# Performance work log

Measured on AMD Instinct MI355X. Metric: run time of the kernel, lower is better.

The kernel has to match this reference:

```python
import jax, jax.numpy as jnp
import numpy as np

N, E = 50000, 300000
NI, EI, H, OUT, L = 16, 8, 64, 3, 3  # node/edge input widths, hidden, output, conv_depth


def setup_inputs() -> dict:
    key = jax.random.key(0)
    ks = iter(jax.random.split(key, 64))
    def rn(shape, scale=0.05):
        return jax.random.normal(next(ks), shape, dtype=jnp.float32) * scale
    inp = {}
    inp["nodes"] = jax.random.normal(next(ks), (N, NI), dtype=jnp.float32)
    inp["edges"] = jax.random.normal(next(ks), (E, EI), dtype=jnp.float32)
    inp["edge_idx"] = jax.random.randint(next(ks), (E, 2), 0, N, dtype=jnp.int32)
    def mlp_params(prefix, din, lead=None):
        s = () if lead is None else (lead,)
        inp[prefix + "_W1"] = rn(s + (din, H))
        inp[prefix + "_b1"] = jnp.zeros(s + (H,), jnp.float32)
        inp[prefix + "_W2"] = rn(s + (H, H))
        inp[prefix + "_b2"] = jnp.zeros(s + (H,), jnp.float32)
        inp[prefix + "_g"] = jnp.ones(s + (H,), jnp.float32)
        inp[prefix + "_be"] = jnp.zeros(s + (H,), jnp.float32)
    mlp_params("ne", NI)            # node encoder
    mlp_params("ee", EI)            # edge encoder
    mlp_params("nm", 2 * H, lead=L)  # node messengers (stacked over conv_depth)
    mlp_params("em", 3 * H, lead=L)  # edge messengers
    inp["dec_W1"] = rn((H, H)); inp["dec_b1"] = jnp.zeros((H,), jnp.float32)
    inp["dec_W2"] = rn((H, OUT)); inp["dec_b2"] = jnp.zeros((OUT,), jnp.float32)
    return inp


def _lrelu(x):
    return jnp.where(x >= 0, x, 0.05 * x)


def _ln(x, g, b):
    m = jnp.mean(x, axis=-1, keepdims=True)
    v = jnp.mean((x - m) ** 2, axis=-1, keepdims=True)
    return (x - m) * jax.lax.rsqrt(v + 1e-5) * g + b


def _mlp(x, W1, b1, W2, b2, g, b):
    h = _lrelu(x @ W1 + b1)
    h = _lrelu(h @ W2 + b2)
    return _ln(h, g, b)


def reference(nodes, edges, edge_idx,
              ne_W1, ne_b1, ne_W2, ne_b2, ne_g, ne_be,
              ee_W1, ee_b1, ee_W2, ee_b2, ee_g, ee_be,
              nm_W1, nm_b1, nm_W2, nm_b2, nm_g, nm_be,
              em_W1, em_b1, em_W2, em_b2, em_g, em_be,
              dec_W1, dec_b1, dec_W2, dec_b2):
    n = _mlp(nodes, ne_W1, ne_b1, ne_W2, ne_b2, ne_g, ne_be)   # [N, H]
    e = _mlp(edges, ee_W1, ee_b1, ee_W2, ee_b2, ee_g, ee_be)   # [E, H]
    s, r = edge_idx[:, 0], edge_idx[:, 1]
    for i in range(L):
        e = e + _mlp(jnp.concatenate([e, n[s], n[r]], axis=1),
                     em_W1[i], em_b1[i], em_W2[i], em_b2[i], em_g[i], em_be[i])
        aggr = jax.ops.segment_sum(e, s, num_segments=n.shape[0])  # scatter_add onto senders
        n = n + _mlp(jnp.concatenate([n, aggr], axis=1),
                     nm_W1[i], nm_b1[i], nm_W2[i], nm_b2[i], nm_g[i], nm_be[i])
    h = _lrelu(n @ dec_W1 + dec_b1)
    return h @ dec_W2 + dec_b2  # [N, OUT]
```

## Files before the change

### kernel.cpp

```cpp
#include <hip/hip_runtime.h>

typedef __attribute__((ext_vector_type(8))) short short8v;
typedef __attribute__((ext_vector_type(4))) short short4v;
typedef __attribute__((ext_vector_type(4))) float f32x4;

__device__ __forceinline__ float lrelu(float x) { return x >= 0.f ? x : 0.05f * x; }

__device__ __forceinline__ unsigned short bf16_rne(float x) {
    unsigned u = __float_as_uint(x);
    u += 0x7FFFu + ((u >> 16) & 1u);
    return (unsigned short)(u >> 16);
}
__device__ __forceinline__ float bf16_to_f(unsigned short h) {
    return __uint_as_float(((unsigned)h) << 16);
}
__device__ __forceinline__ void split2(float x, unsigned short& hi, unsigned short& lo) {
    hi = bf16_rne(x);
    lo = bf16_rne(x - bf16_to_f(hi));
}


__device__ __forceinline__ void stageW(const float* src, int row0, int nrows,
                                       short* __restrict__ A, int wm, int lane)
{
    #pragma unroll
    for (int it = 0; it < 4; ++it) {
        const int q = it * 64 + lane;
        const int rl = wm * 16 + (q >> 4);
        const int k0 = (q & 15) << 2;
        const int grow = row0 + rl;
        float4 x = (grow < nrows) ? *reinterpret_cast<const float4*>(src + (long long)grow * 64 + k0)
                                  : make_float4(0.f, 0.f, 0.f, 0.f);
        unsigned short h0,h1,h2,h3,l0,l1,l2,l3;
        split2(x.x, h0, l0); split2(x.y, h1, l1); split2(x.z, h2, l2); split2(x.w, h3, l3);
        const int off = rl * 64 + ((((k0 >> 3) ^ (rl & 7))) << 3) + (k0 & 7);
        short4v hv; hv[0]=(short)h0; hv[1]=(short)h1; hv[2]=(short)h2; hv[3]=(short)h3;
        short4v lv; lv[0]=(short)l0; lv[1]=(short)l1; lv[2]=(short)l2; lv[3]=(short)l3;
        *reinterpret_cast<short4v*>(A + off) = hv;
        *reinterpret_cast<short4v*>(A + 4096 + off) = lv;
    }
}

__device__ __forceinline__ void gemm64(const short* __restrict__ A, const short* __restrict__ wf,
                                       int row, int g, int lane, f32x4* __restrict__ acc)
{
    #pragma unroll
    for (int s = 0; s < 2; ++s) {
        const int k8 = s * 4 + g;
        const int aoff = row * 64 + ((k8 ^ (row & 7)) << 3);
        const short8v a_hi = *reinterpret_cast<const short8v*>(A + aoff);
        const short8v a_lo = *reinterpret_cast<const short8v*>(A + 4096 + aoff);
        #pragma unroll
        for (int t = 0; t < 4; ++t) {
            const short8v b_hi = *reinterpret_cast<const short8v*>(wf + ((s*4+t)*2+0)*512 + lane*8);
            const short8v b_lo = *reinterpret_cast<const short8v*>(wf + ((s*4+t)*2+1)*512 + lane*8);
            acc[t] = __builtin_amdgcn_mfma_f32_16x16x32_bf16(a_hi, b_hi, acc[t], 0, 0, 0);
            acc[t] = __builtin_amdgcn_mfma_f32_16x16x32_bf16(a_lo, b_hi, acc[t], 0, 0, 0);
            acc[t] = __builtin_amdgcn_mfma_f32_16x16x32_bf16(a_hi, b_lo, acc[t], 0, 0, 0);
        }
    }
}

__device__ __forceinline__ void repackW(short* __restrict__ A, const float4* __restrict__ q,
                                        int wm, int g, int c4)
{
    #pragma unroll
    for (int r = 0; r < 4; ++r) {
        const int rl = wm * 16 + g * 4 + r;
        const int off = rl * 64 + (((c4 >> 3) ^ (rl & 7)) << 3) + (c4 & 7);
        unsigned short h0,h1,h2,h3,l0,l1,l2,l3;
        split2(q[r].x, h0, l0); split2(q[r].y, h1, l1); split2(q[r].z, h2, l2); split2(q[r].w, h3, l3);
        short4v hv; hv[0]=(short)h0; hv[1]=(short)h1; hv[2]=(short)h2; hv[3]=(short)h3;
        short4v lv; lv[0]=(short)l0; lv[1]=(short)l1; lv[2]=(short)l2; lv[3]=(short)l3;
        *reinterpret_cast<short4v*>(A + off) = hv;
        *reinterpret_cast<short4v*>(A + 4096 + off) = lv;
    }
}

__global__ void k_prepw(const float* __restrict__ emW1, const float* __restrict__ emW2,
                        const float* __restrict__ nmW1, const float* __restrict__ nmW2,
                        const float* __restrict__ eeW2, const float* __restrict__ neW2,
                        const float* __restrict__ decW1,
                        short* __restrict__ wf)
{
    const int cid = blockIdx.x;
    const float* src;
    if (cid < 21) {
        const int layer = cid / 7, j = cid % 7;
        src =
            j == 0 ? emW1 + (size_t)layer * 12288 :
            j == 1 ? emW1 + (size_t)layer * 12288 + 4096 :
            j == 2 ? emW1 + (size_t)layer * 12288 + 8192 :
            j == 3 ? emW2 + (size_t)layer * 4096 :
            j == 4 ? nmW1 + (size_t)layer * 8192 :
            j == 5 ? nmW1 + (size_t)layer * 8192 + 4096 :
                     nmW2 + (size_t)layer * 4096;
    } else {
        src = (cid == 21) ? eeW2 : (cid == 22) ? neW2 : decW1;
    }
    short* dst = wf + (size_t)cid * 8192;
    for (int fr = threadIdx.x; fr < 1024; fr += 256) {
        const int lane = fr & 63;
        const int stp = fr >> 6;
        const int p = stp & 1;
        const int st = stp >> 1;
        const int s = st >> 2, t = st & 3;
        const int col = ((lane & 15) << 2) + t;
        const int k0 = s * 32 + (lane >> 4) * 8;
        short8v o;
        #pragma unroll
        for (int i = 0; i < 8; ++i) {
            const float w = src[(k0 + i) * 64 + col];
            const unsigned short hi = bf16_rne(w);
            o[i] = (short)(p ? bf16_rne(w - bf16_to_f(hi)) : hi);
        }
        *reinterpret_cast<short8v*>(dst + fr * 8) = o;
    }
}

template<int DIN, bool PERM, bool MAKEUV, bool OUTBF16>
__global__ __launch_bounds__(256, 4) void k_enc_mf(
    const float* __restrict__ x, const int* __restrict__ csr,
    const float* __restrict__ W1, const float* __restrict__ b1,
    const short* __restrict__ wfW2, const float* __restrict__ b2,
    const float* __restrict__ gam, const float* __restrict__ bet,
    float* __restrict__ out,
    const short* __restrict__ wfB, const short* __restrict__ wfC,
    float* __restrict__ u, float* __restrict__ v, int nrows)
{
    __shared__ short Hf[8192];
    const int row0 = blockIdx.x * 64;
    const int lane = threadIdx.x & 63;
    const int wm = threadIdx.x >> 6;
    const int g = lane >> 4, c = lane & 15;
    const int c4 = c << 2;
    const int rowA = wm * 16 + c;

    long long orig[4];
    #pragma unroll
    for (int r = 0; r < 4; ++r) {
        const int grow = row0 + wm * 16 + g * 4 + r;
        orig[r] = (grow < nrows) ? (long long)(PERM ? csr[grow] : grow) : -1;
    }

    const f32x4 z4 = {0.f, 0.f, 0.f, 0.f};
    f32x4 acc[4];
    #pragma unroll
    for (int t = 0; t < 4; ++t) acc[t] = z4;

    #pragma unroll
    for (int kq = 0; kq < DIN / 4; ++kq) {
        float xv[4][4];
        #pragma unroll
        for (int r = 0; r < 4; ++r) {
            float4 t4 = make_float4(0.f, 0.f, 0.f, 0.f);
            if (orig[r] >= 0)
                t4 = *reinterpret_cast<const float4*>(x + orig[r] * DIN + kq * 4);
            xv[r][0] = t4.x; xv[r][1] = t4.y; xv[r][2] = t4.z; xv[r][3] = t4.w;
        }
        #pragma unroll
        for (int i = 0; i < 4; ++i) {
            const int k = kq * 4 + i;
            const float4 w4 = *reinterpret_cast<const float4*>(W1 + k * 64 + c4);
            const float wv[4] = {w4.x, w4.y, w4.z, w4.w};
            #pragma unroll
            for (int t = 0; t < 4; ++t)
                #pragma unroll
                for (int r = 0; r < 4; ++r)
                    acc[t][r] = fmaf(xv[r][i], wv[t], acc[t][r]);
        }
    }

    const float4 b1q = *reinterpret_cast<const float4*>(b1 + c4);
    float4 hq[4];
    #pragma unroll
    for (int r = 0; r < 4; ++r) {
        hq[r].x = lrelu(acc[0][r] + b1q.x);
        hq[r].y = lrelu(acc[1][r] + b1q.y);
        hq[r].z = lrelu(acc[2][r] + b1q.z);
        hq[r].w = lrelu(acc[3][r] + b1q.w);
    }
    repackW(Hf, hq, wm, g, c4);
    __builtin_amdgcn_wave_barrier();

    f32x4 acc2[4];
    #pragma unroll
    for (int t = 0; t < 4; ++t) acc2[t] = z4;
    gemm64(Hf, wfW2, rowA, g, lane, acc2);

    const float4 b2q = *reinterpret_cast<const float4*>(b2 + c4);
    const float b2a[4] = {b2q.x, b2q.y, b2q.z, b2q.w};
    #pragma unroll
    for (int t = 0; t < 4; ++t) {
        #pragma unroll
        for (int r = 0; r < 4; ++r) acc2[t][r] = lrelu(acc2[t][r] + b2a[t]);
    }
    const float4 gq = *reinterpret_cast<const float4*>(gam + c4);
    const float4 bq = *reinterpret_cast<const float4*>(bet + c4);
    float4 nq[4];
    #pragma unroll
    for (int r = 0; r < 4; ++r) {
        float s = acc2[0][r] + acc2[1][r] + acc2[2][r] + acc2[3][r];
        s += __shfl_xor(s, 1); s += __shfl_xor(s, 2); s += __shfl_xor(s, 4); s += __shfl_xor(s, 8);
        const float mu = s * 0.015625f;
        float q = 0.f;
        #pragma unroll
        for (int t = 0; t < 4; ++t) { const float d = acc2[t][r] - mu; q = fmaf(d, d, q); }
        q += __shfl_xor(q, 1); q += __shfl_xor(q, 2); q += __shfl_xor(q, 4); q += __shfl_xor(q, 8);
        const float rs = rsqrtf(q * 0.015625f + 1e-5f);
        nq[r].x = (acc2[0][r] - mu) * rs * gq.x + bq.x;
        nq[r].y = (acc2[1][r] - mu) * rs * gq.y + bq.y;
        nq[r].z = (acc2[2][r] - mu) * rs * gq.z + bq.z;
        nq[r].w = (acc2[3][r] - mu) * rs * gq.w + bq.w;
        const int grow = row0 + wm * 16 + g * 4 + r;
        if (grow < nrows) {
            if constexpr (OUTBF16) {
                short4v st;
                st[0] = (short)bf16_rne(nq[r].x);
                st[1] = (short)bf16_rne(nq[r].y);
                st[2] = (short)bf16_rne(nq[r].z);
                st[3] = (short)bf16_rne(nq[r].w);
                *reinterpret_cast<short4v*>(reinterpret_cast<unsigned short*>(out) + (long long)grow * 64 + c4) = st;
            } else {
                *reinterpret_cast<float4*>(out + (long long)grow * 64 + c4) = nq[r];
            }
        }
    }

    if constexpr (MAKEUV) {
        repackW(Hf, nq, wm, g, c4);
        __builtin_amdgcn_wave_barrier();
        #pragma unroll
        for (int t = 0; t < 4; ++t) acc2[t] = z4;
        gemm64(Hf, wfB, rowA, g, lane, acc2);
        #pragma unroll
        for (int r = 0; r < 4; ++r) {
            const int grow = row0 + wm * 16 + g * 4 + r;
            if (grow < nrows) {
                float4 o; o.x = acc2[0][r]; o.y = acc2[1][r]; o.z = acc2[2][r]; o.w = acc2[3][r];
                *reinterpret_cast<float4*>(u + (long long)grow * 64 + c4) = o;
            }
        }
        #pragma unroll
        for (int t = 0; t < 4; ++t) acc2[t] = z4;
        gemm64(Hf, wfC, rowA, g, lane, acc2);
        #pragma unroll
        for (int r = 0; r < 4; ++r) {
            const int grow = row0 + wm * 16 + g * 4 + r;
            if (grow < nrows) {
                float4 o; o.x = acc2[0][r]; o.y = acc2[1][r]; o.z = acc2[2][r]; o.w = acc2[3][r];
                *reinterpret_cast<float4*>(v + (long long)grow * 64 + c4) = o;
            }
        }
    }
}

__global__ __launch_bounds__(256, 4) void k_edge_mf(
    unsigned short* ebf, const int* __restrict__ sp, const int* __restrict__ rp,
    const float* __restrict__ u, const float* __restrict__ v,
    const short* __restrict__ wfA, const short* __restrict__ wfW2,
    const float* __restrict__ b1, const float* __restrict__ b2,
    const float* __restrict__ gam, const float* __restrict__ bet, int E)
{
    __shared__ short Hf[8192];
    const int row0 = blockIdx.x * 64;
    const int lane = threadIdx.x & 63;
    const int wm = threadIdx.x >> 6;
    const int g = lane >> 4, c = lane & 15;
    const int c4 = c << 2;
    const int rowA = wm * 16 + c;

    int sidx[4], ridx[4];
    #pragma unroll
    for (int r = 0; r < 4; ++r) {
        const int grow = row0 + wm * 16 + g * 4 + r;
        if (grow < E) { sidx[r] = sp[grow]; ridx[r] = rp[grow]; }
        else          { sidx[r] = 0; ridx[r] = 0; }
    }
    const int arow = (row0 + rowA < E) ? row0 + rowA : 0;
    const short8v a0 = *reinterpret_cast<const short8v*>(ebf + (long long)arow * 64 + g * 8);
    const short8v a1 = *reinterpret_cast<const short8v*>(ebf + (long long)arow * 64 + 32 + g * 8);
    short4v eold[4];
    #pragma unroll
    for (int r = 0; r < 4; ++r) {
        const int grow = row0 + wm * 16 + g * 4 + r;
        const int rc = (grow < E) ? grow : 0;
        eold[r] = *reinterpret_cast<const short4v*>(ebf + (long long)rc * 64 + c4);
    }
    float4 uu[4], vv[4];
    #pragma unroll
    for (int r = 0; r < 4; ++r) {
        uu[r] = *reinterpret_cast<const float4*>(u + (long long)sidx[r] * 64 + c4);
        vv[r] = *reinterpret_cast<const float4*>(v + (long long)ridx[r] * 64 + c4);
    }

    const f32x4 z4 = {0.f, 0.f, 0.f, 0.f};
    f32x4 acc[4];
    #pragma unroll
    for (int t = 0; t < 4; ++t) acc[t] = z4;
    #pragma unroll
    for (int s = 0; s < 2; ++s) {
        const short8v a = s ? a1 : a0;
        #pragma unroll
        for (int t = 0; t < 4; ++t) {
            const short8v b_hi = *reinterpret_cast<const short8v*>(wfA + ((s*4+t)*2+0)*512 + lane*8);
            const short8v b_lo = *reinterpret_cast<const short8v*>(wfA + ((s*4+t)*2+1)*512 + lane*8);
            acc[t] = __builtin_amdgcn_mfma_f32_16x16x32_bf16(a, b_hi, acc[t], 0, 0, 0);
            acc[t] = __builtin_amdgcn_mfma_f32_16x16x32_bf16(a, b_lo, acc[t], 0, 0, 0);
        }
    }

    const float4 b1q = *reinterpret_cast<const float4*>(b1 + c4);
    float4 hq[4];
    #pragma unroll
    for (int r = 0; r < 4; ++r) {
        hq[r].x = lrelu(acc[0][r] + b1q.x + uu[r].x + vv[r].x);
        hq[r].y = lrelu(acc[1][r] + b1q.y + uu[r].y + vv[r].y);
        hq[r].z = lrelu(acc[2][r] + b1q.z + uu[r].z + vv[r].z);
        hq[r].w = lrelu(acc[3][r] + b1q.w + uu[r].w + vv[r].w);
    }
    repackW(Hf, hq, wm, g, c4);
    __builtin_amdgcn_wave_barrier();

    f32x4 acc2[4];
    #pragma unroll
    for (int t = 0; t < 4; ++t) acc2[t] = z4;
    gemm64(Hf, wfW2, rowA, g, lane, acc2);

    const float4 b2q = *reinterpret_cast<const float4*>(b2 + c4);
    const float b2a[4] = {b2q.x, b2q.y, b2q.z, b2q.w};
    #pragma unroll
    for (int t = 0; t < 4; ++t) {
        #pragma unroll
        for (int r = 0; r < 4; ++r) acc2[t][r] = lrelu(acc2[t][r] + b2a[t]);
    }
    const float4 gq = *reinterpret_cast<const float4*>(gam + c4);
    const float4 bq = *reinterpret_cast<const float4*>(bet + c4);
    #pragma unroll
    for (int r = 0; r < 4; ++r) {
        float s = acc2[0][r] + acc2[1][r] + acc2[2][r] + acc2[3][r];
        s += __shfl_xor(s, 1); s += __shfl_xor(s, 2); s += __shfl_xor(s, 4); s += __shfl_xor(s, 8);
        const float mu = s * 0.015625f;
        float q = 0.f;
        #pragma unroll
        for (int t = 0; t < 4; ++t) { const float d = acc2[t][r] - mu; q = fmaf(d, d, q); }
        q += __shfl_xor(q, 1); q += __shfl_xor(q, 2); q += __shfl_xor(q, 4); q += __shfl_xor(q, 8);
        const float rs = rsqrtf(q * 0.015625f + 1e-5f);
        const int grow = row0 + wm * 16 + g * 4 + r;
        if (grow < E) {
            float ox = (acc2[0][r] - mu) * rs * gq.x + bq.x + bf16_to_f((unsigned short)eold[r][0]);
            float oy = (acc2[1][r] - mu) * rs * gq.y + bq.y + bf16_to_f((unsigned short)eold[r][1]);
            float oz = (acc2[2][r] - mu) * rs * gq.z + bq.z + bf16_to_f((unsigned short)eold[r][2]);
            float ow = (acc2[3][r] - mu) * rs * gq.w + bq.w + bf16_to_f((unsigned short)eold[r][3]);
            short4v st;
            st[0] = (short)bf16_rne(ox);
            st[1] = (short)bf16_rne(oy);
            st[2] = (short)bf16_rne(oz);
            st[3] = (short)bf16_rne(ow);
            *reinterpret_cast<short4v*>(ebf + (long long)grow * 64 + c4) = st;
        }
    }
}

__global__ __launch_bounds__(256) void k_aggr(
    const unsigned short* __restrict__ ebf, const int* __restrict__ starts,
    const int* __restrict__ cnt, float* __restrict__ aggr, int N)
{
    const int node = blockIdx.x * 4 + (threadIdx.x >> 6);
    if (node >= N) return;
    const int j = threadIdx.x & 63;
    const int st = starts[node], en = st + cnt[node];
    float a = 0.f;
    for (int t = st; t < en; ++t)
        a += bf16_to_f(ebf[(long long)t * 64 + j]);
    aggr[(long long)node * 64 + j] = a;
}

__global__ __launch_bounds__(256, 4) void k_node_mf(
    float* n, const float* aggr,
    const short* __restrict__ wfW1a, const short* __restrict__ wfW1b, const short* __restrict__ wfW2,
    const float* __restrict__ b1, const float* __restrict__ b2,
    const float* __restrict__ gam, const float* __restrict__ bet,
    const short* __restrict__ wfB, const short* __restrict__ wfC,
    float* u, float* v, int N)
{
    __shared__ short An[8192];
    __shared__ short Aa[8192];
    const int row0 = blockIdx.x * 64;
    const int lane = threadIdx.x & 63;
    const int wm = threadIdx.x >> 6;
    const int g = lane >> 4, c = lane & 15;
    const int c4 = c << 2;
    const int rowA = wm * 16 + c;

    stageW(n, row0, N, An, wm, lane);
    stageW(aggr, row0, N, Aa, wm, lane);
    __builtin_amdgcn_wave_barrier();

    const f32x4 z4 = {0.f, 0.f, 0.f, 0.f};
    f32x4 acc[4];
    #pragma unroll
    for (int t = 0; t < 4; ++t) acc[t] = z4;
    gemm64(An, wfW1a, rowA, g, lane, acc);
    gemm64(Aa, wfW1b, rowA, g, lane, acc);

    const float4 b1q = *reinterpret_cast<const float4*>(b1 + c4);
    float4 hq[4];
    #pragma unroll
    for (int r = 0; r < 4; ++r) {
        hq[r].x = lrelu(acc[0][r] + b1q.x);
        hq[r].y = lrelu(acc[1][r] + b1q.y);
        hq[r].z = lrelu(acc[2][r] + b1q.z);
        hq[r].w = lrelu(acc[3][r] + b1q.w);
    }
    __builtin_amdgcn_wave_barrier();
    repackW(Aa, hq, wm, g, c4);
    __builtin_amdgcn_wave_barrier();

    f32x4 acc2[4];
    #pragma unroll
    for (int t = 0; t < 4; ++t) acc2[t] = z4;
    gemm64(Aa, wfW2, rowA, g, lane, acc2);

    const float4 b2q = *reinterpret_cast<const float4*>(b2 + c4);
    const float b2a[4] = {b2q.x, b2q.y, b2q.z, b2q.w};
    #pragma unroll
    for (int t = 0; t < 4; ++t) {
        #pragma unroll
        for (int r = 0; r < 4; ++r) acc2[t][r] = lrelu(acc2[t][r] + b2a[t]);
    }
    const float4 gq = *reinterpret_cast<const float4*>(gam + c4);
    const float4 bq = *reinterpret_cast<const float4*>(bet + c4);
    float4 nq[4];
    #pragma unroll
    for (int r = 0; r < 4; ++r) {
        float s = acc2[0][r] + acc2[1][r] + acc2[2][r] + acc2[3][r];
        s += __shfl_xor(s, 1); s += __shfl_xor(s, 2); s += __shfl_xor(s, 4); s += __shfl_xor(s, 8);
        const float mu = s * 0.015625f;
        float q = 0.f;
        #pragma unroll
        for (int t = 0; t < 4; ++t) { const float d = acc2[t][r] - mu; q = fmaf(d, d, q); }
        q += __shfl_xor(q, 1); q += __shfl_xor(q, 2); q += __shfl_xor(q, 4); q += __shfl_xor(q, 8);
        const float rs = rsqrtf(q * 0.015625f + 1e-5f);
        const int rl = wm * 16 + g * 4 + r;
        const int off = rl * 64 + (((c4 >> 3) ^ (rl & 7)) << 3) + (c4 & 7);
        const short4v nh = *reinterpret_cast<const short4v*>(An + off);
        const short4v nl = *reinterpret_cast<const short4v*>(An + 4096 + off);
        nq[r].x = (acc2[0][r] - mu) * rs * gq.x + bq.x + bf16_to_f((unsigned short)nh[0]) + bf16_to_f((unsigned short)nl[0]);
        nq[r].y = (acc2[1][r] - mu) * rs * gq.y + bq.y + bf16_to_f((unsigned short)nh[1]) + bf16_to_f((unsigned short)nl[1]);
        nq[r].z = (acc2[2][r] - mu) * rs * gq.z + bq.z + bf16_to_f((unsigned short)nh[2]) + bf16_to_f((unsigned short)nl[2]);
        nq[r].w = (acc2[3][r] - mu) * rs * gq.w + bq.w + bf16_to_f((unsigned short)nh[3]) + bf16_to_f((unsigned short)nl[3]);
        const int grow = row0 + rl;
        if (grow < N)
            *reinterpret_cast<float4*>(n + (long long)grow * 64 + c4) = nq[r];
    }

    if (wfB) {
        __builtin_amdgcn_wave_barrier();
        repackW(An, nq, wm, g, c4);
        __builtin_amdgcn_wave_barrier();
        #pragma unroll
        for (int t = 0; t < 4; ++t) acc2[t] = z4;
        gemm64(An, wfB, rowA, g, lane, acc2);
        #pragma unroll
        for (int r = 0; r < 4; ++r) {
            const int grow = row0 + wm * 16 + g * 4 + r;
            if (grow < N) {
                float4 o; o.x = acc2[0][r]; o.y = acc2[1][r]; o.z = acc2[2][r]; o.w = acc2[3][r];
                *reinterpret_cast<float4*>(u + (long long)grow * 64 + c4) = o;
            }
        }
        #pragma unroll
        for (int t = 0; t < 4; ++t) acc2[t] = z4;
        gemm64(An, wfC, rowA, g, lane, acc2);
        #pragma unroll
        for (int r = 0; r < 4; ++r) {
            const int grow = row0 + wm * 16 + g * 4 + r;
            if (grow < N) {
                float4 o; o.x = acc2[0][r]; o.y = acc2[1][r]; o.z = acc2[2][r]; o.w = acc2[3][r];
                *reinterpret_cast<float4*>(v + (long long)grow * 64 + c4) = o;
            }
        }
    }
}

__global__ __launch_bounds__(256, 4) void k_dec_mf(
    const float* __restrict__ n, const short* __restrict__ wfW1, const float* __restrict__ b1,
    const float* __restrict__ W2, const float* __restrict__ b2,
    float* __restrict__ out, int N)
{
    __shared__ short An[8192];
    const int row0 = blockIdx.x * 64;
    const int lane = threadIdx.x & 63;
    const int wm = threadIdx.x >> 6;
    const int g = lane >> 4, c = lane & 15;
    const int c4 = c << 2;
    const int rowA = wm * 16 + c;
    stageW(n, row0, N, An, wm, lane);
    __builtin_amdgcn_wave_barrier();
    const f32x4 z4 = {0.f, 0.f, 0.f, 0.f};
    f32x4 acc[4];
    #pragma unroll
    for (int t = 0; t < 4; ++t) acc[t] = z4;
    gemm64(An, wfW1, rowA, g, lane, acc);
    const float4 b1q = *reinterpret_cast<const float4*>(b1 + c4);
    const float b1a[4] = {b1q.x, b1q.y, b1q.z, b1q.w};
    #pragma unroll
    for (int t = 0; t < 4; ++t)
        #pragma unroll
        for (int r = 0; r < 4; ++r) acc[t][r] = lrelu(acc[t][r] + b1a[t]);
    const float4 w0 = *reinterpret_cast<const float4*>(W2 + c4 * 3);
    const float4 w1 = *reinterpret_cast<const float4*>(W2 + c4 * 3 + 4);
    const float4 w2 = *reinterpret_cast<const float4*>(W2 + c4 * 3 + 8);
    const float wv[12] = {w0.x,w0.y,w0.z,w0.w, w1.x,w1.y,w1.z,w1.w, w2.x,w2.y,w2.z,w2.w};
    float po[4][3];
    #pragma unroll
    for (int r = 0; r < 4; ++r)
        #pragma unroll
        for (int o = 0; o < 3; ++o)
            po[r][o] = acc[0][r]*wv[o] + acc[1][r]*wv[3+o] + acc[2][r]*wv[6+o] + acc[3][r]*wv[9+o];
    #pragma unroll
    for (int m = 1; m <= 8; m <<= 1)
        #pragma unroll
        for (int r = 0; r < 4; ++r)
            #pragma unroll
            for (int o = 0; o < 3; ++o)
                po[r][o] += __shfl_xor(po[r][o], m);
    if (c < 3) {
        #pragma unroll
        for (int r = 0; r < 4; ++r) {
            const int grow = row0 + wm * 16 + g * 4 + r;
            const float val = (c == 0) ? po[r][0] : (c == 1) ? po[r][1] : po[r][2];
            if (grow < N) out[(long long)grow * 3 + c] = b2[c] + val;
        }
    }
}

__global__ void k_hist(const int* __restrict__ eidx, int* __restrict__ cnt, int E)
{
    int i = blockIdx.x * 256 + threadIdx.x;
    if (i < E) atomicAdd(&cnt[eidx[2 * i]], 1);
}

__global__ void k_scan1(const int* __restrict__ cnt, int* __restrict__ starts,
                        int* __restrict__ bsum, int n)
{
    __shared__ int sh[256];
    const int tid = threadIdx.x;
    const int i = blockIdx.x * 256 + tid;
    const int val = (i < n) ? cnt[i] : 0;
    sh[tid] = val; __syncthreads();
    for (int off = 1; off < 256; off <<= 1) {
        int t = (tid >= off) ? sh[tid - off] : 0;
        __syncthreads();
        sh[tid] += t;
        __syncthreads();
    }
    if (i < n) starts[i] = sh[tid] - val;
    if (tid == 255) bsum[blockIdx.x] = sh[255];
}

__global__ void k_scan2(int* __restrict__ bsum, int nb)
{
    __shared__ int sh[256];
    const int tid = threadIdx.x;
    const int val = (tid < nb) ? bsum[tid] : 0;
    sh[tid] = val; __syncthreads();
    for (int off = 1; off < 256; off <<= 1) {
        int t = (tid >= off) ? sh[tid - off] : 0;
        __syncthreads();
        sh[tid] += t;
        __syncthreads();
    }
    if (tid < nb) bsum[tid] = sh[tid] - val;
}

__global__ void k_scan3(int* __restrict__ starts, const int* __restrict__ bsum, int n)
{
    int i = blockIdx.x * 256 + threadIdx.x;
    if (i < n) starts[i] += bsum[blockIdx.x];
}

__global__ void k_scatter(const int* __restrict__ eidx, const int* __restrict__ starts,
                          int* __restrict__ cursor, int* __restrict__ csr,
                          int* __restrict__ sp, int* __restrict__ rp, int E)
{
    int i = blockIdx.x * 256 + threadIdx.x;
    if (i < E) {
        const int s = eidx[2 * i];
        const int p = atomicAdd(&cursor[s], 1);
        const int q = starts[s] + p;
        csr[q] = i;
        sp[q] = s;
        rp[q] = eidx[2 * i + 1];
    }
}

extern "C" void kernel_launch(void* const* d_in, const int* in_sizes, int n_in,
                              void* d_out, int out_size, void* d_ws, size_t ws_size,
                              hipStream_t stream)
{
    (void)in_sizes; (void)n_in; (void)out_size; (void)ws_size;
    constexpr int N = 50000, E = 300000, L = 3;

    const float* nodes = (const float*)d_in[0];
    const float* edges = (const float*)d_in[1];
    const int*   eidx  = (const int*)d_in[2];
    const float* neW1 = (const float*)d_in[3];
    const float* neb1 = (const float*)d_in[4];
    const float* neW2 = (const float*)d_in[5];
    const float* neb2 = (const float*)d_in[6];
    const float* neg  = (const float*)d_in[7];
    const float* nebe = (const float*)d_in[8];
    const float* eeW1 = (const float*)d_in[9];
    const float* eeb1 = (const float*)d_in[10];
    const float* eeW2 = (const float*)d_in[11];
    const float* eeb2 = (const float*)d_in[12];
    const float* eeg  = (const float*)d_in[13];
    const float* eebe = (const float*)d_in[14];
    const float* nmW1 = (const float*)d_in[15];
    const float* nmb1 = (const float*)d_in[16];
    const float* nmW2 = (const float*)d_in[17];
    const float* nmb2 = (const float*)d_in[18];
    const float* nmg  = (const float*)d_in[19];
    const float* nmbe = (const float*)d_in[20];
    const float* emW1 = (const float*)d_in[21];
    const float* emb1 = (const float*)d_in[22];
    const float* emW2 = (const float*)d_in[23];
    const float* emb2 = (const float*)d_in[24];
    const float* emg  = (const float*)d_in[25];
    const float* embe = (const float*)d_in[26];
    const float* decW1 = (const float*)d_in[27];
    const float* decb1 = (const float*)d_in[28];
    const float* decW2 = (const float*)d_in[29];
    const float* decb2 = (const float*)d_in[30];

    float* n   = (float*)d_ws;
    float* u   = n + (size_t)N * 64;
    float* v   = u + (size_t)N * 64;
    int* cnt    = (int*)(v + (size_t)N * 64);
    int* starts = cnt + N;
    int* csr    = starts + N;
    int* bsum   = csr + E;
    int* cursor = bsum + 256;
    int* sp     = cursor + N;
    int* rp     = sp + E;
    short* wf   = (short*)(rp + E);
    unsigned short* ebf = (unsigned short*)(wf + (size_t)24 * 8192);

    const int nbN = (N + 255) / 256;
    const int nbE = (E + 255) / 256;
    const int nbN64 = (N + 63) / 64;
    const int nbE64 = (E + 63) / 64;

    const short* wfEE  = wf + (size_t)21 * 8192;
    const short* wfNE  = wf + (size_t)22 * 8192;
    const short* wfDec = wf + (size_t)23 * 8192;

    k_prepw<<<24, 256, 0, stream>>>(emW1, emW2, nmW1, nmW2, eeW2, neW2, decW1, wf);
    hipMemsetAsync(cnt, 0, (size_t)N * sizeof(int), stream);
    hipMemsetAsync(cursor, 0, (size_t)N * sizeof(int), stream);
    k_hist<<<nbE, 256, 0, stream>>>(eidx, cnt, E);
    k_scan1<<<nbN, 256, 0, stream>>>(cnt, starts, bsum, N);
    k_scan2<<<1, 256, 0, stream>>>(bsum, nbN);
    k_scan3<<<nbN, 256, 0, stream>>>(starts, bsum, N);
    k_scatter<<<nbE, 256, 0, stream>>>(eidx, starts, cursor, csr, sp, rp, E);

    const short* wl0 = wf;
    k_enc_mf<16, false, true, false><<<nbN64, 256, 0, stream>>>(
        nodes, nullptr, neW1, neb1, wfNE, neb2, neg, nebe, n,
        wl0 + 8192, wl0 + 2 * 8192, u, v, N);
    k_enc_mf<8, true, false, true><<<nbE64, 256, 0, stream>>>(
        edges, csr, eeW1, eeb1, wfEE, eeb2, eeg, eebe, (float*)ebf,
        nullptr, nullptr, nullptr, nullptr, E);

    for (int i = 0; i < L; ++i) {
        const short* wl = wf + (size_t)i * 7 * 8192;
        k_edge_mf<<<nbE64, 256, 0, stream>>>(ebf, sp, rp, u, v, wl, wl + 3 * 8192,
                                             emb1 + i * 64, emb2 + i * 64,
                                             emg + i * 64, embe + i * 64, E);
        k_aggr<<<(N + 3) / 4, 256, 0, stream>>>(ebf, starts, cnt, u, N);
        const short* wln = (i + 1 < L) ? wf + (size_t)(i + 1) * 7 * 8192 : nullptr;
        k_node_mf<<<nbN64, 256, 0, stream>>>(n, u,
                                             wl + 4 * 8192, wl + 5 * 8192, wl + 6 * 8192,
                                             nmb1 + i * 64, nmb2 + i * 64,
                                             nmg + i * 64, nmbe + i * 64,
                                             wln ? wln + 8192 : nullptr,
                                             wln ? wln + 2 * 8192 : nullptr,
                                             u, v, N);
    }
    k_dec_mf<<<nbN64, 256, 0, stream>>>(n, wfDec, decb1, decW2, decb2, (float*)d_out, N);
}
```

Baseline: 425.6 us.

## Process four edge tiles per block with software-pipelined gathers in edge kernel

```diff
diff --git a/kernel.cpp b/kernel.cpp
--- a/kernel.cpp
+++ b/kernel.cpp
@@ -263,101 +263,127 @@
     const float* __restrict__ gam, const float* __restrict__ bet, int E)
 {
     __shared__ short Hf[8192];
-    const int row0 = blockIdx.x * 64;
+    const int base = blockIdx.x * 256;
     const int lane = threadIdx.x & 63;
     const int wm = threadIdx.x >> 6;
     const int g = lane >> 4, c = lane & 15;
     const int c4 = c << 2;
     const int rowA = wm * 16 + c;
 
-    int sidx[4], ridx[4];
-    #pragma unroll
-    for (int r = 0; r < 4; ++r) {
-        const int grow = row0 + wm * 16 + g * 4 + r;
-        if (grow < E) { sidx[r] = sp[grow]; ridx[r] = rp[grow]; }
-        else          { sidx[r] = 0; ridx[r] = 0; }
-    }
-    const int arow = (row0 + rowA < E) ? row0 + rowA : 0;
-    const short8v a0 = *reinterpret_cast<const short8v*>(ebf + (long long)arow * 64 + g * 8);
-    const short8v a1 = *reinterpret_cast<const short8v*>(ebf + (long long)arow * 64 + 32 + g * 8);
-    short4v eold[4];
-    #pragma unroll
-    for (int r = 0; r < 4; ++r) {
-        const int grow = row0 + wm * 16 + g * 4 + r;
-        const int rc = (grow < E) ? grow : 0;
-        eold[r] = *reinterpret_cast<const short4v*>(ebf + (long long)rc * 64 + c4);
-    }
-    float4 uu[4], vv[4];
-    #pragma unroll
-    for (int r = 0; r < 4; ++r) {
-        uu[r] = *reinterpret_cast<const float4*>(u + (long long)sidx[r] * 64 + c4);
-        vv[r] = *reinterpret_cast<const float4*>(v + (long long)ridx[r] * 64 + c4);
-    }
+    const float4 b1q = *reinterpret_cast<const float4*>(b1 + c4);
+    const float4 b2q = *reinterpret_cast<const float4*>(b2 + c4);
+    const float4 gq  = *reinterpret_cast<const float4*>(gam + c4);
+    const float4 bq  = *reinterpret_cast<const float4*>(bet + c4);
+
+    auto loadIdx = [&](int t, int* si, int* ri) {
+        #pragma unroll
+        for (int r = 0; r < 4; ++r) {
+            const int grow = base + t * 64 + wm * 16 + g * 4 + r;
+            if (grow < E) { si[r] = sp[grow]; ri[r] = rp[grow]; }
+            else          { si[r] = 0; ri[r] = 0; }
+        }
+    };
+    auto loadA = [&](int t, short8v& a0, short8v& a1) {
+        const int arow = (base + t * 64 + rowA < E) ? base + t * 64 + rowA : 0;
+        a0 = *reinterpret_cast<const short8v*>(ebf + (long long)arow * 64 + g * 8);
+        a1 = *reinterpret_cast<const short8v*>(ebf + (long long)arow * 64 + 32 + g * 8);
+    };
+    auto gather = [&](const int* si, const int* ri, float4* uu, float4* vv) {
+        #pragma unroll
+        for (int r = 0; r < 4; ++r) {
+            uu[r] = *reinterpret_cast<const float4*>(u + (long long)si[r] * 64 + c4);
+            vv[r] = *reinterpret_cast<const float4*>(v + (long long)ri[r] * 64 + c4);
+        }
+    };
+
+    int si[4][4], ri[4][4];
+    short8v a0v[4], a1v[4];
+    float4 uuv[4][4], vvv[4][4];
+
+    loadIdx(0, si[0], ri[0]);
+    loadIdx(1, si[1], ri[1]);
+    loadA(0, a0v[0], a1v[0]);
+    gather(si[0], ri[0], uuv[0], vvv[0]);
 
     const f32x4 z4 = {0.f, 0.f, 0.f, 0.f};
-    f32x4 acc[4];
-    #pragma unroll
-    for (int t = 0; t < 4; ++t) acc[t] = z4;
-    #pragma unroll
-    for (int s = 0; s < 2; ++s) {
-        const short8v a = s ? a1 : a0;
-        #pragma unroll
-        for (int t = 0; t < 4; ++t) {
-            const short8v b_hi = *reinterpret_cast<const short8v*>(wfA + ((s*4+t)*2+0)*512 + lane*8);
-            const short8v b_lo = *reinterpret_cast<const short8v*>(wfA + ((s*4+t)*2+1)*512 + lane*8);
-            acc[t] = __builtin_amdgcn_mfma_f32_16x16x32_bf16(a, b_hi, acc[t], 0, 0, 0);
-            acc[t] = __builtin_amdgcn_mfma_f32_16x16x32_bf16(a, b_lo, acc[t], 0, 0, 0);
-        }
-    }
-
-    const float4 b1q = *reinterpret_cast<const float4*>(b1 + c4);
-    float4 hq[4];
-    #pragma unroll
-    for (int r = 0; r < 4; ++r) {
-        hq[r].x = lrelu(acc[0][r] + b1q.x + uu[r].x + vv[r].x);
-        hq[r].y = lrelu(acc[1][r] + b1q.y + uu[r].y + vv[r].y);
-        hq[r].z = lrelu(acc[2][r] + b1q.z + uu[r].z + vv[r].z);
-        hq[r].w = lrelu(acc[3][r] + b1q.w + uu[r].w + vv[r].w);
-    }
-    repackW(Hf, hq, wm, g, c4);
-    __builtin_amdgcn_wave_barrier();
-
-    f32x4 acc2[4];
-    #pragma unroll
-    for (int t = 0; t < 4; ++t) acc2[t] = z4;
-    gemm64(Hf, wfW2, rowA, g, lane, acc2);
-
-    const float4 b2q = *reinterpret_cast<const float4*>(b2 + c4);
-    const float b2a[4] = {b2q.x, b2q.y, b2q.z, b2q.w};
+
     #pragma unroll
     for (int t = 0; t < 4; ++t) {
-        #pragma unroll
-        for (int r = 0; r < 4; ++r) acc2[t][r] = lrelu(acc2[t][r] + b2a[t]);
-    }
-    const float4 gq = *reinterpret_cast<const float4*>(gam + c4);
-    const float4 bq = *reinterpret_cast<const float4*>(bet + c4);
-    #pragma unroll
-    for (int r = 0; r < 4; ++r) {
-        float s = acc2[0][r] + acc2[1][r] + acc2[2][r] + acc2[3][r];
-        s += __shfl_xor(s, 1); s += __shfl_xor(s, 2); s += __shfl_xor(s, 4); s += __shfl_xor(s, 8);
-        const float mu = s * 0.015625f;
-        float q = 0.f;
-        #pragma unroll
-        for (int t = 0; t < 4; ++t) { const float d = acc2[t][r] - mu; q = fmaf(d, d, q); }
-        q += __shfl_xor(q, 1); q += __shfl_xor(q, 2); q += __shfl_xor(q, 4); q += __shfl_xor(q, 8);
-        const float rs = rsqrtf(q * 0.015625f + 1e-5f);
-        const int grow = row0 + wm * 16 + g * 4 + r;
-        if (grow < E) {
-            float ox = (acc2[0][r] - mu) * rs * gq.x + bq.x + bf16_to_f((unsigned short)eold[r][0]);
-            float oy = (acc2[1][r] - mu) * rs * gq.y + bq.y + bf16_to_f((unsigned short)eold[r][1]);
-            float oz = (acc2[2][r] - mu) * rs * gq.z + bq.z + bf16_to_f((unsigned short)eold[r][2]);
-            float ow = (acc2[3][r] - mu) * rs * gq.w + bq.w + bf16_to_f((unsigned short)eold[r][3]);
-            short4v st;
-            st[0] = (short)bf16_rne(ox);
-            st[1] = (short)bf16_rne(oy);
-            st[2] = (short)bf16_rne(oz);
-            st[3] = (short)bf16_rne(ow);
-            *reinterpret_cast<short4v*>(ebf + (long long)grow * 64 + c4) = st;
+        if (t + 2 < 4) loadIdx(t + 2, si[t + 2], ri[t + 2]);
+        if (t + 1 < 4) {
+            loadA(t + 1, a0v[t + 1], a1v[t + 1]);
+            gather(si[t + 1], ri[t + 1], uuv[t + 1], vvv[t + 1]);
+        }
+
+        f32x4 acc[4];
+        #pragma unroll
+        for (int q = 0; q < 4; ++q) acc[q] = z4;
+        #pragma unroll
+        for (int s = 0; s < 2; ++s) {
+            const short8v a = s ? a1v[t] : a0v[t];
+            #pragma unroll
+            for (int q = 0; q < 4; ++q) {
+                const short8v b_hi = *reinterpret_cast<const short8v*>(wfA + ((s*4+q)*2+0)*512 + lane*8);
+                const short8v b_lo = *reinterpret_cast<const short8v*>(wfA + ((s*4+q)*2+1)*512 + lane*8);
+                acc[q] = __builtin_amdgcn_mfma_f32_16x16x32_bf16(a, b_hi, acc[q], 0, 0, 0);
+                acc[q] = __builtin_amdgcn_mfma_f32_16x16x32_bf16(a, b_lo, acc[q], 0, 0, 0);
+            }
+        }
+
+        float4 hq[4];
+        #pragma unroll
+        for (int r = 0; r < 4; ++r) {
+            hq[r].x = lrelu(acc[0][r] + b1q.x + uuv[t][r].x + vvv[t][r].x);
+            hq[r].y = lrelu(acc[1][r] + b1q.y + uuv[t][r].y + vvv[t][r].y);
+            hq[r].z = lrelu(acc[2][r] + b1q.z + uuv[t][r].z + vvv[t][r].z);
+            hq[r].w = lrelu(acc[3][r] + b1q.w + uuv[t][r].w + vvv[t][r].w);
+        }
+        repackW(Hf, hq, wm, g, c4);
+        __builtin_amdgcn_wave_barrier();
+
+        short4v eold[4];
+        #pragma unroll
+        for (int r = 0; r < 4; ++r) {
+            const int grow = base + t * 64 + wm * 16 + g * 4 + r;
+            const int rc = (grow < E) ? grow : 0;
+            eold[r] = *reinterpret_cast<const short4v*>(ebf + (long long)rc * 64 + c4);
+        }
+
+        f32x4 acc2[4];
+        #pragma unroll
+        for (int q = 0; q < 4; ++q) acc2[q] = z4;
+        gemm64(Hf, wfW2, rowA, g, lane, acc2);
+        __builtin_amdgcn_wave_barrier();
+
+        #pragma unroll
+        for (int q = 0; q < 4; ++q) {
+            const float bb = (q == 0) ? b2q.x : (q == 1) ? b2q.y : (q == 2) ? b2q.z : b2q.w;
+            #pragma unroll
+            for (int r = 0; r < 4; ++r) acc2[q][r] = lrelu(acc2[q][r] + bb);
+        }
+        #pragma unroll
+        for (int r = 0; r < 4; ++r) {
+            float s = acc2[0][r] + acc2[1][r] + acc2[2][r] + acc2[3][r];
+            s += __shfl_xor(s, 1); s += __shfl_xor(s, 2); s += __shfl_xor(s, 4); s += __shfl_xor(s, 8);
+            const float mu = s * 0.015625f;
+            float q2 = 0.f;
+            #pragma unroll
+            for (int q = 0; q < 4; ++q) { const float d = acc2[q][r] - mu; q2 = fmaf(d, d, q2); }
+            q2 += __shfl_xor(q2, 1); q2 += __shfl_xor(q2, 2); q2 += __shfl_xor(q2, 4); q2 += __shfl_xor(q2, 8);
+            const float rs = rsqrtf(q2 * 0.015625f + 1e-5f);
+            const int grow = base + t * 64 + wm * 16 + g * 4 + r;
+            if (grow < E) {
+                const float ox = (acc2[0][r] - mu) * rs * gq.x + bq.x + bf16_to_f((unsigned short)eold[r][0]);
+                const float oy = (acc2[1][r] - mu) * rs * gq.y + bq.y + bf16_to_f((unsigned short)eold[r][1]);
+                const float oz = (acc2[2][r] - mu) * rs * gq.z + bq.z + bf16_to_f((unsigned short)eold[r][2]);
+                const float ow = (acc2[3][r] - mu) * rs * gq.w + bq.w + bf16_to_f((unsigned short)eold[r][3]);
+                short4v st;
+                st[0] = (short)bf16_rne(ox);
+                st[1] = (short)bf16_rne(oy);
+                st[2] = (short)bf16_rne(oz);
+                st[3] = (short)bf16_rne(ow);
+                *reinterpret_cast<short4v*>(ebf + (long long)grow * 64 + c4) = st;
+            }
         }
     }
 }
@@ -652,6 +678,7 @@
     const int nbE = (E + 255) / 256;
     const int nbN64 = (N + 63) / 64;
     const int nbE64 = (E + 63) / 64;
+    const int nbE256 = (E + 255) / 256;
 
     const short* wfEE  = wf + (size_t)21 * 8192;
     const short* wfNE  = wf + (size_t)22 * 8192;
@@ -676,9 +703,9 @@
 
     for (int i = 0; i < L; ++i) {
         const short* wl = wf + (size_t)i * 7 * 8192;
-        k_edge_mf<<<nbE64, 256, 0, stream>>>(ebf, sp, rp, u, v, wl, wl + 3 * 8192,
-                                             emb1 + i * 64, emb2 + i * 64,
-                                             emg + i * 64, embe + i * 64, E);
+        k_edge_mf<<<nbE256, 256, 0, stream>>>(ebf, sp, rp, u, v, wl, wl + 3 * 8192,
+                                              emb1 + i * 64, emb2 + i * 64,
+                                              emg + i * 64, embe + i * 64, E);
         k_aggr<<<(N + 3) / 4, 256, 0, stream>>>(ebf, starts, cnt, u, N);
         const short* wln = (i + 1 < L) ? wf + (size_t)(i + 1) * 7 * 8192 : nullptr;
         k_node_mf<<<nbN64, 256, 0, stream>>>(n, u,
```

After: 1.110 ms. +160.9%, slower.
